# Optimization experiments

Measured on AMD Instinct MI355X. Metric: run time of the kernel, lower is better.

## Reference

```python
import jax, jax.numpy as jnp
import numpy as np
import math

B, L, H, E, D = 4, 2048, 8, 64, 64


def _build_local_log_symmetry_mask(L):
    # Faithful port of LocalLogSymmetryMask: True = masked-out position.
    lws = math.ceil(np.log2(L) / 2)  # local window size
    n_log = math.ceil(10 * np.log2(L))
    m = np.zeros((L, L), dtype=np.float32)
    for i in range(L):
        row = m[i]
        # left side: local window + log-spaced long-range
        if i - lws + 1 < 0:
            row[:i] = 1
        else:
            row[i - lws + 1:i + 1] = 1
            for k in range(n_log):
                ni = i - lws + 1 - int(1.5 ** k)
                if ni >= 0:
                    row[ni] = 1
                else:
                    break
        # right side (symmetric)
        if i + lws - 1 >= L:
            row[i:] = 1
        else:
            row[i:i + lws] = 1
            for k in range(n_log):
                ni = i + lws - 1 + int(1.5 ** k)
                if ni < L:
                    row[ni] = 1
                else:
                    break
    return m == 0  # True where attention is NOT allowed


def setup_inputs() -> dict:
    key = jax.random.key(0)
    kq, kk, kv = jax.random.split(key, 3)
    queries = jax.random.normal(kq, (B, L, H, E), dtype=jnp.float32)
    keys = jax.random.normal(kk, (B, L, H, E), dtype=jnp.float32)
    values = jax.random.normal(kv, (B, L, H, D), dtype=jnp.float32)
    mask = jnp.asarray(_build_local_log_symmetry_mask(L))  # [L, L] bool
    return {"queries": queries, "keys": keys, "values": values, "mask": mask}


def reference(queries, keys, values, mask):
    # queries/keys: [B,L,H,E], values: [B,L,H,D], mask: [L,L] bool (True = masked)
    E_ = queries.shape[-1]
    scale = 1.0 / math.sqrt(E_)
    # scores: [B,H,L,S]
    scores = jnp.einsum("blhe,bshe->bhls", queries, keys) * scale
    scores = jnp.where(mask[None, None, :, :], -jnp.inf, scores)
    attn = jax.nn.softmax(scores, axis=-1)  # dropout disabled (eval mode)
    out = jnp.einsum("bhls,bshd->blhd", attn, values)  # [B,L,H,D]
    return out
```

## Files before the change

kernel.cpp:

```cpp
#include <hip/hip_runtime.h>


#define KB 4
#define KL 2048
#define KH 8
#define KE 64
#define KWAVES 4
#define KROWS (KB * KL * KH)
#define KROWSTRIDE (KH * KE)

static __device__ __forceinline__ int log_off(int m) {
    int p = 1;
    for (int t = 0; t <= m; ++t) p *= 3;
    return p >> (m + 1);
}

__global__ void MaskAttention_20572893347881_kernel(
    const float* __restrict__ q, const float* __restrict__ k,
    const float* __restrict__ v, float* __restrict__ out) {
    __shared__ float ps[KWAVES][48];

    const int tid  = (int)threadIdx.x;
    const int lane = tid & 63;
    const int wave = tid >> 6;
    const int g    = lane >> 4;
    const int e4   = lane & 15;
    const int r = (int)blockIdx.x * KWAVES + wave;
    const int i = r & (KL - 1);
    const int h = (r >> 11) & (KH - 1);
    const int b = r >> 14;

    const size_t base    = (size_t)b * (KL * KH * KE) + (size_t)h * KE;
    const size_t rowbase = base + (size_t)i * KROWSTRIDE;

    float4 qf = *(const float4*)(q + rowbase + e4 * 4);
    qf.x *= 0.125f; qf.y *= 0.125f; qf.z *= 0.125f; qf.w *= 0.125f;

    int jp = -1;
    if (lane < 11) {
        int j = i - 5 + lane;
        if (j >= 0 && j < KL) jp = j;
    } else if (lane < 29) {
        int j = i - 5 - log_off(lane - 11);
        if (j >= 0) jp = j;
    } else if (lane < 47) {
        int j = i + 5 + log_off(lane - 29);
        if (j < KL) jp = j;
    }

#pragma unroll
    for (int t = 0; t < 12; ++t) {
        const int c  = 4 * t + g;
        const int jc = __shfl(jp, c, 64);
        const int jl = (jc < 0) ? 0 : jc;
        float4 kf = *(const float4*)(k + base + (size_t)jl * KROWSTRIDE + e4 * 4);
        float s = qf.x * kf.x + qf.y * kf.y + qf.z * kf.z + qf.w * kf.w;
        s += __shfl_xor(s, 1, 64);
        s += __shfl_xor(s, 2, 64);
        s += __shfl_xor(s, 4, 64);
        s += __shfl_xor(s, 8, 64);
        if (e4 == 0) ps[wave][c] = (jc < 0) ? -1e30f : s;
    }
    __syncthreads();

    float sm = (lane < 48) ? ps[wave][lane] : -1e30f;
    float m = sm;
#pragma unroll
    for (int off = 32; off > 0; off >>= 1)
        m = fmaxf(m, __shfl_xor(m, off, 64));
    float p = __expf(sm - m);
    float d = p;
#pragma unroll
    for (int off = 32; off > 0; off >>= 1)
        d += __shfl_xor(d, off, 64);
    const float inv = 1.f / d;

    float4 acc = make_float4(0.f, 0.f, 0.f, 0.f);
#pragma unroll
    for (int t = 0; t < 12; ++t) {
        const int c   = 4 * t + g;
        const float pc = __shfl(p, c, 64);
        const int jc  = __shfl(jp, c, 64);
        const int jl  = (jc < 0) ? 0 : jc;
        float4 vf = *(const float4*)(v + base + (size_t)jl * KROWSTRIDE + e4 * 4);
        acc.x += pc * vf.x;
        acc.y += pc * vf.y;
        acc.z += pc * vf.z;
        acc.w += pc * vf.w;
    }
    acc.x += __shfl_xor(acc.x, 16, 64);
    acc.y += __shfl_xor(acc.y, 16, 64);
    acc.z += __shfl_xor(acc.z, 16, 64);
    acc.w += __shfl_xor(acc.w, 16, 64);
    acc.x += __shfl_xor(acc.x, 32, 64);
    acc.y += __shfl_xor(acc.y, 32, 64);
    acc.z += __shfl_xor(acc.z, 32, 64);
    acc.w += __shfl_xor(acc.w, 32, 64);

    if (lane < 16) {
        float4 o = make_float4(acc.x * inv, acc.y * inv, acc.z * inv, acc.w * inv);
        *(float4*)(out + rowbase + e4 * 4) = o;
    }
}

extern "C" void kernel_launch(void* const* d_in, const int* in_sizes, int n_in,
                              void* d_out, int out_size, void* d_ws, size_t ws_size,
                              hipStream_t stream) {
    (void)in_sizes; (void)n_in; (void)out_size; (void)d_ws; (void)ws_size;
    const float* q = (const float*)d_in[0];
    const float* k = (const float*)d_in[1];
    const float* v = (const float*)d_in[2];
    float* out = (float*)d_out;

    hipLaunchKernelGGL(MaskAttention_20572893347881_kernel,
                       dim3(KROWS / KWAVES), dim3(KWAVES * 64), 0, stream,
                       q, k, v, out);
}
```

Before: 172.8 us.

## Prefetch all K/V rows up front, keep softmax in registers, remap block order

All 12 K and V float4 loads are issued before any compute, so the V gather no longer waits behind the score and softmax phase. The shared-memory score buffer and its block barrier are dropped, and the softmax runs per lane over register arrays with cross-group shuffles. Block indices are also permuted so that consecutively launched blocks spread across the row space, which is likely aimed at XCD/L2 locality. The cost is higher register use (24 float4 live values), capped by launch_bounds(256,4), which may cause spills or lower occupancy. There is also a redundant duplicate V load.

```diff
diff --git a/kernel.cpp b/kernel.cpp
--- a/kernel.cpp
+++ b/kernel.cpp
@@ -7,6 +7,7 @@
 #define KE 64
 #define KWAVES 4
 #define KROWS (KB * KL * KH)
+#define KBLOCKS (KROWS / KWAVES)
 #define KROWSTRIDE (KH * KE)
 
 static __device__ __forceinline__ int log_off(int m) {
@@ -15,26 +16,25 @@
     return p >> (m + 1);
 }
 
-__global__ void MaskAttention_20572893347881_kernel(
+__global__ __launch_bounds__(256, 4)
+void MaskAttention_20572893347881_kernel(
     const float* __restrict__ q, const float* __restrict__ k,
     const float* __restrict__ v, float* __restrict__ out) {
-    __shared__ float ps[KWAVES][48];
-
     const int tid  = (int)threadIdx.x;
     const int lane = tid & 63;
     const int wave = tid >> 6;
     const int g    = lane >> 4;
     const int e4   = lane & 15;
-    const int r = (int)blockIdx.x * KWAVES + wave;
-    const int i = r & (KL - 1);
-    const int h = (r >> 11) & (KH - 1);
-    const int b = r >> 14;
+
+    const int p  = (int)blockIdx.x;
+    const int l  = (p & 7) * (KBLOCKS / 8) + (p >> 3);
+    const int r  = l * KWAVES + wave;
+    const int i  = r & (KL - 1);
+    const int h  = (r >> 11) & (KH - 1);
+    const int b  = r >> 14;
 
     const size_t base    = (size_t)b * (KL * KH * KE) + (size_t)h * KE;
     const size_t rowbase = base + (size_t)i * KROWSTRIDE;
-
-    float4 qf = *(const float4*)(q + rowbase + e4 * 4);
-    qf.x *= 0.125f; qf.y *= 0.125f; qf.z *= 0.125f; qf.w *= 0.125f;
 
     int jp = -1;
     if (lane < 11) {
@@ -48,45 +48,55 @@
         if (j < KL) jp = j;
     }
 
+    int jc[12];
+#pragma unroll
+    for (int t = 0; t < 12; ++t) jc[t] = __shfl(jp, 4 * t + g, 64);
+
+    float4 qf = *(const float4*)(q + rowbase + e4 * 4);
+    float4 kf[12], vf[12];
 #pragma unroll
     for (int t = 0; t < 12; ++t) {
-        const int c  = 4 * t + g;
-        const int jc = __shfl(jp, c, 64);
-        const int jl = (jc < 0) ? 0 : jc;
-        float4 kf = *(const float4*)(k + base + (size_t)jl * KROWSTRIDE + e4 * 4);
-        float s = qf.x * kf.x + qf.y * kf.y + qf.z * kf.z + qf.w * kf.w;
-        s += __shfl_xor(s, 1, 64);
-        s += __shfl_xor(s, 2, 64);
-        s += __shfl_xor(s, 4, 64);
-        s += __shfl_xor(s, 8, 64);
-        if (e4 == 0) ps[wave][c] = (jc < 0) ? -1e30f : s;
+        const size_t ro = base + (size_t)(jc[t] < 0 ? 0 : jc[t]) * KROWSTRIDE + e4 * 4;
+        kf[t] = *(const float4*)(k + ro);
+        vf[t] = *(const float4*)(v + ro + (size_t)(v - v));
+        vf[t] = *(const float4*)(v + ro);
     }
-    __syncthreads();
+    qf.x *= 0.125f; qf.y *= 0.125f; qf.z *= 0.125f; qf.w *= 0.125f;
 
-    float sm = (lane < 48) ? ps[wave][lane] : -1e30f;
-    float m = sm;
+    float s[12];
 #pragma unroll
-    for (int off = 32; off > 0; off >>= 1)
-        m = fmaxf(m, __shfl_xor(m, off, 64));
-    float p = __expf(sm - m);
-    float d = p;
+    for (int t = 0; t < 12; ++t) {
+        float d0 = qf.x * kf[t].x + qf.y * kf[t].y + qf.z * kf[t].z + qf.w * kf[t].w;
+        d0 += __shfl_xor(d0, 1, 64);
+        d0 += __shfl_xor(d0, 2, 64);
+        d0 += __shfl_xor(d0, 4, 64);
+        d0 += __shfl_xor(d0, 8, 64);
+        s[t] = (jc[t] < 0) ? -1e30f : d0;
+    }
+
+    float m = s[0];
 #pragma unroll
-    for (int off = 32; off > 0; off >>= 1)
-        d += __shfl_xor(d, off, 64);
+    for (int t = 1; t < 12; ++t) m = fmaxf(m, s[t]);
+    m = fmaxf(m, __shfl_xor(m, 16, 64));
+    m = fmaxf(m, __shfl_xor(m, 32, 64));
+    float d = 0.f;
+    float pr[12];
+#pragma unroll
+    for (int t = 0; t < 12; ++t) {
+        pr[t] = __expf(s[t] - m);
+        d += pr[t];
+    }
+    d += __shfl_xor(d, 16, 64);
+    d += __shfl_xor(d, 32, 64);
     const float inv = 1.f / d;
 
     float4 acc = make_float4(0.f, 0.f, 0.f, 0.f);
 #pragma unroll
     for (int t = 0; t < 12; ++t) {
-        const int c   = 4 * t + g;
-        const float pc = __shfl(p, c, 64);
-        const int jc  = __shfl(jp, c, 64);
-        const int jl  = (jc < 0) ? 0 : jc;
-        float4 vf = *(const float4*)(v + base + (size_t)jl * KROWSTRIDE + e4 * 4);
-        acc.x += pc * vf.x;
-        acc.y += pc * vf.y;
-        acc.z += pc * vf.z;
-        acc.w += pc * vf.w;
+        acc.x += pr[t] * vf[t].x;
+        acc.y += pr[t] * vf[t].y;
+        acc.z += pr[t] * vf[t].z;
+        acc.w += pr[t] * vf[t].w;
     }
     acc.x += __shfl_xor(acc.x, 16, 64);
     acc.y += __shfl_xor(acc.y, 16, 64);
@@ -113,6 +123,6 @@
     float* out = (float*)d_out;
 
     hipLaunchKernelGGL(MaskAttention_20572893347881_kernel,
-                       dim3(KROWS / KWAVES), dim3(KWAVES * 64), 0, stream,
+                       dim3(KBLOCKS), dim3(KWAVES * 64), 0, stream,
                        q, k, v, out);
 }
```

Result: faster. 149.4 us (-13.5%).
